# Kernel tuning notes

Measured on AMD Instinct MI355X. Metric: run time of the kernel, lower is better.

Reference implementation:

```python
import jax, jax.numpy as jnp
import numpy as np

N = 8192      # nodes
IN = 1433     # input_feat_dim
H1 = 256      # hidden_dim1
H2 = 128      # hidden_dim2
EPS = 1e-5    # BatchNorm1d eps
NEG = -9e15   # GAT mask value
SLOPE = 0.2   # leaky_relu negative slope (gamma)


def setup_inputs() -> dict:
    key = jax.random.key(0)
    ks = jax.random.split(key, 8)
    x = jax.random.normal(ks[0], (N, H2), dtype=jnp.float32)
    u = jax.random.uniform(ks[1], (N, N), dtype=jnp.float32)
    adj = jnp.where(u > 0.999, jnp.float32(0.01), jnp.float32(0.0))
    def w(k, shape):
        fan = shape[0]
        return jax.random.normal(k, shape, dtype=jnp.float32) / jnp.sqrt(jnp.float32(fan))
    return {
        "x": x,
        "adj": adj,
        "W_att": w(ks[2], (H2, H2)),
        "a_att": w(ks[3], (2 * H2, 1)),
        "W_fd1": w(ks[4], (H2, H1)),
        "bn1_g": jnp.ones((H1,), jnp.float32),
        "bn1_b": jnp.zeros((H1,), jnp.float32),
        "W_fd2": w(ks[5], (H1, IN)),
        "bn2_g": jnp.ones((IN,), jnp.float32),
        "bn2_b": jnp.zeros((IN,), jnp.float32),
        "W_sd1": w(ks[6], (H2, H1)),
        "bn3_g": jnp.ones((H1,), jnp.float32),
        "bn3_b": jnp.zeros((H1,), jnp.float32),
    }


def batchnorm(h, g, b):
    # BatchNorm1d training-mode forward: batch stats, biased variance
    m = h.mean(axis=0)
    v = ((h - m) ** 2).mean(axis=0)
    return (h - m) * jax.lax.rsqrt(v + EPS) * g + b


def reference(x, adj, W_att, a_att, W_fd1, bn1_g, bn1_b, W_fd2, bn2_g, bn2_b,
              W_sd1, bn3_g, bn3_b):
    # --- GraphAttentionLayer (concat=False, dropout=0) ---
    Wh = x @ W_att                       # [N, H2]
    f1 = Wh @ a_att[:H2]                 # [N, 1]
    f2 = Wh @ a_att[H2:]                 # [N, 1]
    e = jax.nn.leaky_relu(f1 + f2.T, SLOPE)          # [N, N]
    att = jnp.where(adj > 0, e, jnp.float32(NEG))
    att = jax.nn.softmax(att, axis=1)
    z = att @ Wh                         # condensed encoder output [N, H2]
    # --- feature decoder branch ---
    h1 = jax.nn.relu(adj @ (z @ W_fd1))  # GCN: adj @ (X W), relu
    h1 = batchnorm(h1, bn1_g, bn1_b)
    feat = jax.nn.relu(adj @ (h1 @ W_fd2))
    feat = batchnorm(feat, bn2_g, bn2_b)
    # --- structure decoder branch ---
    s1 = jax.nn.relu(adj @ (z @ W_sd1))
    s1 = batchnorm(s1, bn3_g, bn3_b)
    struct = s1 @ s1.T                   # inner-product decode, identity act [N, N]
    return feat, struct
```

## Files before the change

### kernel.cpp

```cpp
#include <hip/hip_runtime.h>
#include <hip/hip_bf16.h>
#include <stdint.h>

#define NN 8192
#define MAXNZ 64
#define BN_EPS 1e-5f
#define SLOPE 0.2f
#define IND 1433
#define NPAD 1536

typedef float f32x4v __attribute__((ext_vector_type(4)));
typedef short bf16x8v __attribute__((ext_vector_type(8)));

__device__ __forceinline__ float wave_sum(float v) {
#pragma unroll
  for (int off = 32; off > 0; off >>= 1) v += __shfl_xor(v, off);
  return v;
}
__device__ __forceinline__ float wave_max(float v) {
#pragma unroll
  for (int off = 32; off > 0; off >>= 1) v = fmaxf(v, __shfl_xor(v, off));
  return v;
}

#define GLOAD_LDS16(g, l)                                                      \
  __builtin_amdgcn_global_load_lds(                                            \
      (const __attribute__((address_space(1))) unsigned int*)(g),              \
      (__attribute__((address_space(3))) unsigned int*)(l), 16, 0, 0)

__global__ __launch_bounds__(256) void prep_gemm_k(
    const float* __restrict__ A, const float* __restrict__ B,
    const float* __restrict__ aatt, const float* __restrict__ W_fd2,
    const float* __restrict__ W_fd1, const float* __restrict__ W_sd1,
    __hip_bfloat16* __restrict__ Wt, __hip_bfloat16* __restrict__ Wcatb,
    float* __restrict__ C, float* __restrict__ cs, float* __restrict__ f1,
    float* __restrict__ f2) {
  __shared__ float As[64][68];
  __shared__ float Bs[64][68];
  __shared__ float csL[64];
  const int b = blockIdx.x;
  const int t = threadIdx.x;
  if (b < NPAD) {
    int o = b * 256 + t;
    int n = o >> 8, k = o & 255;
    Wt[o] = __float2bfloat16(n < IND ? W_fd2[(size_t)k * IND + n] : 0.f);
    if (b < 256) {
      int nn = o >> 7, kk = o & 127;
      float v = nn < 256 ? W_fd1[(size_t)kk * 256 + nn]
                         : W_sd1[(size_t)kk * 256 + (nn - 256)];
      Wcatb[o] = __float2bfloat16(v);
    }
    return;
  }
  const int bx = b - NPAD;
  const int m0 = (bx & 127) * 64, n0 = (bx >> 7) * 64;
  const int tx = t & 15, ty = t >> 4;
  if (t < 64) csL[t] = 0.f;
  float acc[4][4] = {};
  for (int kt = 0; kt < 128; kt += 64) {
    if (kt) __syncthreads();
#pragma unroll
    for (int i = 0; i < 4; ++i) {
      int fid = t + 256 * i;
      int r = fid >> 4, kq = (fid & 15) * 4;
      float4 v = *(const float4*)&A[(size_t)(m0 + r) * 128 + kt + kq];
      *(float4*)&As[r][kq] = v;
    }
#pragma unroll
    for (int i = 0; i < 4; ++i) {
      int fid = t + 256 * i;
      int r = fid >> 4, cq = (fid & 15) * 4;
      float4 v = *(const float4*)&B[(size_t)(kt + r) * 128 + n0 + cq];
      *(float4*)&Bs[r][cq] = v;
    }
    __syncthreads();
#pragma unroll 4
    for (int k0 = 0; k0 < 64; k0 += 4) {
      float4 a[4], bb[4];
#pragma unroll
      for (int i = 0; i < 4; ++i) a[i] = *(const float4*)&As[ty * 4 + i][k0];
#pragma unroll
      for (int j = 0; j < 4; ++j) bb[j] = *(const float4*)&Bs[k0 + j][tx * 4];
#pragma unroll
      for (int kk = 0; kk < 4; ++kk) {
#pragma unroll
        for (int i = 0; i < 4; ++i) {
          float av = ((const float*)&a[i])[kk];
#pragma unroll
          for (int j = 0; j < 4; ++j)
            acc[i][j] += av * ((const float*)&bb[kk])[j];
        }
      }
    }
  }
#pragma unroll
  for (int i = 0; i < 4; ++i) {
    float4 v = make_float4(acc[i][0], acc[i][1], acc[i][2], acc[i][3]);
    *(float4*)&C[(size_t)(m0 + ty * 4 + i) * 128 + n0 + tx * 4] = v;
  }
  float a1v[4], a2v[4];
#pragma unroll
  for (int j = 0; j < 4; ++j) {
    a1v[j] = aatt[n0 + tx * 4 + j];
    a2v[j] = aatt[128 + n0 + tx * 4 + j];
  }
#pragma unroll
  for (int i = 0; i < 4; ++i) {
    float p1 = acc[i][0] * a1v[0] + acc[i][1] * a1v[1] + acc[i][2] * a1v[2] +
               acc[i][3] * a1v[3];
    float p2 = acc[i][0] * a2v[0] + acc[i][1] * a2v[1] + acc[i][2] * a2v[2] +
               acc[i][3] * a2v[3];
#pragma unroll
    for (int off = 1; off < 16; off <<= 1) {
      p1 += __shfl_xor(p1, off);
      p2 += __shfl_xor(p2, off);
    }
    if ((t & 15) == 0) {
      atomicAdd(&f1[m0 + ty * 4 + i], p1);
      atomicAdd(&f2[m0 + ty * 4 + i], p2);
    }
  }
  float cp[4];
#pragma unroll
  for (int j = 0; j < 4; ++j) {
    cp[j] = acc[0][j] + acc[1][j] + acc[2][j] + acc[3][j];
    cp[j] += __shfl_xor(cp[j], 16);
    cp[j] += __shfl_xor(cp[j], 32);
  }
  if ((t & 63) < 16) {
#pragma unroll
    for (int j = 0; j < 4; ++j) atomicAdd(&csL[(t & 15) * 4 + j], cp[j]);
  }
  __syncthreads();
  if (t < 64) atomicAdd(&cs[n0 + t], csL[t]);
}

__global__ void extract_attn_k(const float* __restrict__ adj, const float* __restrict__ Wh,
                               const float* __restrict__ f1, const float* __restrict__ f2,
                               const float* __restrict__ cs, int* __restrict__ nnzA,
                               int* __restrict__ idxA, float* __restrict__ valA,
                               float* __restrict__ valsumA, float* __restrict__ z) {
  __shared__ int cntL[4];
  __shared__ int idxL[4][MAXNZ];
  __shared__ float valL[4][MAXNZ];
  int l = threadIdx.x & 63, w = threadIdx.x >> 6;
  int i = blockIdx.x * 4 + w;
  if (l == 0) cntL[w] = 0;
  const float* row = adj + (size_t)i * NN;
  for (int it = 0; it < NN / 512; ++it) {
    int c0 = it * 512 + l * 8;
    float4 va = *(const float4*)&row[c0];
    float4 vb = *(const float4*)&row[c0 + 4];
    float mx = fmaxf(fmaxf(fmaxf(va.x, va.y), fmaxf(va.z, va.w)),
                     fmaxf(fmaxf(vb.x, vb.y), fmaxf(vb.z, vb.w)));
    if (mx > 0.f) {
#pragma unroll
      for (int j = 0; j < 4; ++j) {
        float v = ((const float*)&va)[j];
        if (v > 0.f) {
          int s = atomicAdd(&cntL[w], 1);
          if (s < MAXNZ) { idxL[w][s] = c0 + j; valL[w][s] = v; }
        }
      }
#pragma unroll
      for (int j = 0; j < 4; ++j) {
        float v = ((const float*)&vb)[j];
        if (v > 0.f) {
          int s = atomicAdd(&cntL[w], 1);
          if (s < MAXNZ) { idxL[w][s] = c0 + 4 + j; valL[w][s] = v; }
        }
      }
    }
  }
  int nnz = cntL[w];
  nnz = nnz < MAXNZ ? nnz : MAXNZ;
  if (l == 0) nnzA[i] = nnz;

  int c = -1;
  float v = 0.f, att = 0.f;
  if (l < nnz) { c = idxL[w][l]; v = valL[w][l]; }
  idxA[(size_t)i * MAXNZ + l] = (l < nnz) ? c : 0;
  valA[(size_t)i * MAXNZ + l] = v;
  float vs = wave_sum(v);
  if (l == 0) valsumA[i] = vs;

  if (nnz == 0) {
    const float inv = 1.0f / 8192.0f;
    z[(size_t)i * 128 + l] = cs[l] * inv;
    z[(size_t)i * 128 + 64 + l] = cs[64 + l] * inv;
    return;
  }
  float e = -INFINITY;
  if (l < nnz) {
    float u = f1[i] + f2[c];
    e = u >= 0.f ? u : SLOPE * u;
  }
  float mx = wave_max(e);
  float p = (l < nnz) ? expf(e - mx) : 0.f;
  float s = wave_sum(p);
  att = p / s;
  float a0 = 0.f, a1 = 0.f;
  for (int j = 0; j < nnz; ++j) {
    float wt = __shfl(att, j);
    int r = __shfl(c, j);
    a0 += wt * Wh[(size_t)r * 128 + l];
    a1 += wt * Wh[(size_t)r * 128 + 64 + l];
  }
  z[(size_t)i * 128 + l] = a0;
  z[(size_t)i * 128 + 64 + l] = a1;
}

__global__ void gather_z_k(const float* __restrict__ X, const int* __restrict__ nnzA,
                           const int* __restrict__ idxA, const float* __restrict__ valA,
                           __hip_bfloat16* __restrict__ Y) {
  int l = threadIdx.x & 63, w = threadIdx.x >> 6;
  int i = blockIdx.x * 4 + w;
  int nnz = nnzA[i];
  int myi = idxA[(size_t)i * MAXNZ + l];
  float myv = valA[(size_t)i * MAXNZ + l];
  float a0 = 0.f, a1 = 0.f;
  for (int j = 0; j < nnz; ++j) {
    int r = __shfl(myi, j);
    float v = __shfl(myv, j);
    a0 += v * X[(size_t)r * 128 + l];
    a1 += v * X[(size_t)r * 128 + 64 + l];
  }
  Y[(size_t)i * 128 + l] = __float2bfloat16(a0);
  Y[(size_t)i * 128 + 64 + l] = __float2bfloat16(a1);
}

__global__ void s1_gather_k(const __hip_bfloat16* __restrict__ t, const int* __restrict__ nnzA,
                            const int* __restrict__ idxA, const float* __restrict__ valA,
                            const float* __restrict__ valsumA, const float* __restrict__ sums,
                            const float* __restrict__ sumsq, const float* __restrict__ g1,
                            const float* __restrict__ b1, const float* __restrict__ g3,
                            const float* __restrict__ b3, __hip_bfloat16* __restrict__ s1b,
                            __hip_bfloat16* __restrict__ ghb) {
  __shared__ int idxL[MAXNZ];
  __shared__ float valL[MAXNZ];
  int i = blockIdx.x, tt = threadIdx.x;
  int nnz = nnzA[i];
  if (tt < MAXNZ) {
    idxL[tt] = idxA[(size_t)i * MAXNZ + tt];
    valL[tt] = valA[(size_t)i * MAXNZ + tt];
  }
  __syncthreads();
  {
    float m = sums[256 + tt] * (1.f / 8192.f);
    float va = fmaxf(sumsq[256 + tt] * (1.f / 8192.f) - m * m, 0.f);
    float sc = g3[tt] * rsqrtf(va + BN_EPS);
    float sh = b3[tt] - m * sc;
    float v = __bfloat162float(t[(size_t)i * 512 + 256 + tt]) * sc + sh;
    s1b[(size_t)i * 256 + tt] = __float2bfloat16(v);
  }
  float acc = 0.f;
  for (int j = 0; j < nnz; ++j)
    acc += valL[j] * __bfloat162float(t[(size_t)idxL[j] * 512 + tt]);
  float m = sums[tt] * (1.f / 8192.f);
  float va = fmaxf(sumsq[tt] * (1.f / 8192.f) - m * m, 0.f);
  float sc = g1[tt] * rsqrtf(va + BN_EPS);
  float sh = b1[tt] - m * sc;
  ghb[(size_t)i * 256 + tt] = __float2bfloat16(acc * sc + sh * valsumA[i]);
}

__global__ void feat_apply_k(const __hip_bfloat16* __restrict__ fp, const float* __restrict__ sums,
                             const float* __restrict__ sumsq, const float* __restrict__ g,
                             const float* __restrict__ b, float* __restrict__ out) {
  int i = blockIdx.x;
  for (int c = threadIdx.x; c < IND; c += 256) {
    float m = sums[c] * (1.f / 8192.f);
    float va = fmaxf(sumsq[c] * (1.f / 8192.f) - m * m, 0.f);
    float sc = g[c] * rsqrtf(va + BN_EPS);
    float sh = b[c] - m * sc;
    out[(size_t)i * IND + c] = __bfloat162float(fp[(size_t)i * NPAD + c]) * sc + sh;
  }
}

template <int KT>
__global__ __launch_bounds__(256) void mfma_bt_k(const short* __restrict__ A,
                                                 const short* __restrict__ Bt,
                                                 __hip_bfloat16* __restrict__ C, int ldc,
                                                 int gridN, float* __restrict__ sums,
                                                 float* __restrict__ sumsq) {
  __shared__ short lds[2][16384];
  const int nwg = gridDim.x;
  const int cpx = nwg >> 3;
  const int bid = blockIdx.x;
  const int wg = (bid & 7) * cpx + (bid >> 3);
  const int m0 = (wg / gridN) * 128, n0 = (wg % gridN) * 128;
  const int t = threadIdx.x;
  const int l = t & 63, w = t >> 6;
  const int wm = w >> 1, wn = w & 1;
  const int KW = KT * 128;
  f32x4v acc[4][4];
#pragma unroll
  for (int i = 0; i < 4; ++i)
#pragma unroll
    for (int j = 0; j < 4; ++j)
#pragma unroll
      for (int q = 0; q < 4; ++q) acc[i][j][q] = 0.f;

  for (int kt = 0; kt < KT; ++kt) {
    if (kt) __syncthreads();
#pragma unroll
    for (int i = 0; i < 8; ++i) {
      int region = w * 8 + i;
      int lr = region * 4 + (l >> 4);
      int ch = (l & 15) ^ (lr & 7);
      const short* gA = A + ((size_t)(m0 + lr) * KW + kt * 128 + ch * 8);
      GLOAD_LDS16(gA, &lds[0][region * 512]);
      const short* gB = Bt + ((size_t)(n0 + lr) * KW + kt * 128 + ch * 8);
      GLOAD_LDS16(gB, &lds[1][region * 512]);
    }
    __syncthreads();
#pragma unroll
    for (int ks = 0; ks < 4; ++ks) {
      bf16x8v af[4], bf[4];
#pragma unroll
      for (int mi = 0; mi < 4; ++mi) {
        int lr = wm * 64 + mi * 16 + (l & 15);
        int ch = (ks * 4 + (l >> 4)) ^ (lr & 7);
        af[mi] = *(const bf16x8v*)&lds[0][lr * 128 + ch * 8];
      }
#pragma unroll
      for (int nj = 0; nj < 4; ++nj) {
        int lr = wn * 64 + nj * 16 + (l & 15);
        int ch = (ks * 4 + (l >> 4)) ^ (lr & 7);
        bf[nj] = *(const bf16x8v*)&lds[1][lr * 128 + ch * 8];
      }
#pragma unroll
      for (int mi = 0; mi < 4; ++mi)
#pragma unroll
        for (int nj = 0; nj < 4; ++nj)
          acc[mi][nj] = __builtin_amdgcn_mfma_f32_16x16x32_bf16(
              af[mi], bf[nj], acc[mi][nj], 0, 0, 0);
    }
  }
#pragma unroll
  for (int nj = 0; nj < 4; ++nj) {
    int col = n0 + wn * 64 + nj * 16 + (l & 15);
    float s = 0.f, ss = 0.f;
#pragma unroll
    for (int mi = 0; mi < 4; ++mi) {
#pragma unroll
      for (int q = 0; q < 4; ++q) {
        int row = m0 + wm * 64 + mi * 16 + (l >> 4) * 4 + q;
        float v = fmaxf(acc[mi][nj][q], 0.f);
        C[(size_t)row * ldc + col] = __float2bfloat16(v);
        s += v;
        ss += v * v;
      }
    }
    s += __shfl_xor(s, 16);
    s += __shfl_xor(s, 32);
    ss += __shfl_xor(ss, 16);
    ss += __shfl_xor(ss, 32);
    if ((l >> 4) == 0) {
      atomicAdd(&sums[col], s);
      atomicAdd(&sumsq[col], ss);
    }
  }
}

__global__ __launch_bounds__(256) void tail_k(const short* __restrict__ Agh,
                                              const short* __restrict__ Wt,
                                              __hip_bfloat16* __restrict__ featb,
                                              float* __restrict__ sums,
                                              float* __restrict__ sumsq,
                                              const short* __restrict__ S,
                                              float* __restrict__ C) {
  __shared__ short lds[2][16384];
  const int bid = blockIdx.x;
  const int fA = bid * 24 / 89;
  const int fB = (bid + 1) * 24 / 89;
  const bool isFeat = fB > fA;
  const int t = threadIdx.x;
  const int l = t & 63, w = t >> 6;
  const int wm = w >> 1, wn = w & 1;
  f32x4v acc[4][4];
#pragma unroll
  for (int i = 0; i < 4; ++i)
#pragma unroll
    for (int j = 0; j < 4; ++j)
#pragma unroll
      for (int q = 0; q < 4; ++q) acc[i][j][q] = 0.f;

  if (isFeat) {
    const int fb = fA;
    const int wg = (fb & 7) * 96 + (fb >> 3);
    const int m0 = (wg / 12) * 128, n0 = (wg % 12) * 128;
    for (int kt = 0; kt < 2; ++kt) {
      if (kt) __syncthreads();
#pragma unroll
      for (int i = 0; i < 8; ++i) {
        int region = w * 8 + i;
        int lr = region * 4 + (l >> 4);
        int ch = (l & 15) ^ (lr & 7);
        const short* gA = Agh + ((size_t)(m0 + lr) * 256 + kt * 128 + ch * 8);
        GLOAD_LDS16(gA, &lds[0][region * 512]);
        const short* gB = Wt + ((size_t)(n0 + lr) * 256 + kt * 128 + ch * 8);
        GLOAD_LDS16(gB, &lds[1][region * 512]);
      }
      __syncthreads();
#pragma unroll
      for (int ks = 0; ks < 4; ++ks) {
        bf16x8v af[4], bf[4];
#pragma unroll
        for (int mi = 0; mi < 4; ++mi) {
          int lr = wm * 64 + mi * 16 + (l & 15);
          int ch = (ks * 4 + (l >> 4)) ^ (lr & 7);
          af[mi] = *(const bf16x8v*)&lds[0][lr * 128 + ch * 8];
        }
#pragma unroll
        for (int nj = 0; nj < 4; ++nj) {
          int lr = wn * 64 + nj * 16 + (l & 15);
          int ch = (ks * 4 + (l >> 4)) ^ (lr & 7);
          bf[nj] = *(const bf16x8v*)&lds[1][lr * 128 + ch * 8];
        }
#pragma unroll
        for (int mi = 0; mi < 4; ++mi)
#pragma unroll
          for (int nj = 0; nj < 4; ++nj)
            acc[mi][nj] = __builtin_amdgcn_mfma_f32_16x16x32_bf16(
                af[mi], bf[nj], acc[mi][nj], 0, 0, 0);
      }
    }
#pragma unroll
    for (int nj = 0; nj < 4; ++nj) {
      int col = n0 + wn * 64 + nj * 16 + (l & 15);
      float s = 0.f, ss = 0.f;
#pragma unroll
      for (int mi = 0; mi < 4; ++mi) {
#pragma unroll
        for (int q = 0; q < 4; ++q) {
          int row = m0 + wm * 64 + mi * 16 + (l >> 4) * 4 + q;
          float v = fmaxf(acc[mi][nj][q], 0.f);
          featb[(size_t)row * NPAD + col] = __float2bfloat16(v);
          s += v;
          ss += v * v;
        }
      }
      s += __shfl_xor(s, 16);
      s += __shfl_xor(s, 32);
      ss += __shfl_xor(ss, 16);
      ss += __shfl_xor(ss, 32);
      if ((l >> 4) == 0) {
        atomicAdd(&sums[col], s);
        atomicAdd(&sumsq[col], ss);
      }
    }
  } else {
    const int sb = bid - fA;
    const int wg = (sb & 7) * 260 + (sb >> 3);
    int bi = (int)((129.0f - sqrtf(16641.0f - 8.0f * (float)wg)) * 0.5f);
    while ((bi + 1) * 64 - ((bi + 1) * bi) / 2 <= wg) ++bi;
    while (bi * 64 - (bi * (bi - 1)) / 2 > wg) --bi;
    const int bj = bi + (wg - (bi * 64 - (bi * (bi - 1)) / 2));
    const int m0 = bi * 128, n0 = bj * 128;
    for (int kt = 0; kt < 2; ++kt) {
      if (kt) __syncthreads();
#pragma unroll
      for (int i = 0; i < 8; ++i) {
        int region = w * 8 + i;
        int lr = region * 4 + (l >> 4);
        int ch = (l & 15) ^ (lr & 7);
        const short* gA = S + ((size_t)(m0 + lr) * 256 + kt * 128 + ch * 8);
        GLOAD_LDS16(gA, &lds[0][region * 512]);
        const short* gB = S + ((size_t)(n0 + lr) * 256 + kt * 128 + ch * 8);
        GLOAD_LDS16(gB, &lds[1][region * 512]);
      }
      __syncthreads();
#pragma unroll
      for (int ks = 0; ks < 4; ++ks) {
        bf16x8v af[4], bf[4];
#pragma unroll
        for (int mi = 0; mi < 4; ++mi) {
          int lr = wm * 64 + mi * 16 + (l & 15);
          int ch = (ks * 4 + (l >> 4)) ^ (lr & 7);
          af[mi] = *(const bf16x8v*)&lds[0][lr * 128 + ch * 8];
        }
#pragma unroll
        for (int nj = 0; nj < 4; ++nj) {
          int lr = wn * 64 + nj * 16 + (l & 15);
          int ch = (ks * 4 + (l >> 4)) ^ (lr & 7);
          bf[nj] = *(const bf16x8v*)&lds[1][lr * 128 + ch * 8];
        }
#pragma unroll
        for (int mi = 0; mi < 4; ++mi)
#pragma unroll
          for (int nj = 0; nj < 4; ++nj)
            acc[mi][nj] = __builtin_amdgcn_mfma_f32_16x16x32_bf16(
                af[mi], bf[nj], acc[mi][nj], 0, 0, 0);
      }
    }
#pragma unroll
    for (int mi = 0; mi < 4; ++mi) {
#pragma unroll
      for (int nj = 0; nj < 4; ++nj) {
        int col = n0 + wn * 64 + nj * 16 + (l & 15);
#pragma unroll
        for (int q = 0; q < 4; ++q) {
          int row = m0 + wm * 64 + mi * 16 + (l >> 4) * 4 + q;
          C[(size_t)row * NN + col] = acc[mi][nj][q];
        }
      }
    }
    if (bi != bj) {
#pragma unroll
      for (int nj = 0; nj < 4; ++nj) {
        int col = n0 + wn * 64 + nj * 16 + (l & 15);
#pragma unroll
        for (int mi = 0; mi < 4; ++mi) {
          int row0 = m0 + wm * 64 + mi * 16 + (l >> 4) * 4;
          float4 v = make_float4(acc[mi][nj][0], acc[mi][nj][1], acc[mi][nj][2],
                                 acc[mi][nj][3]);
          *(float4*)&C[(size_t)col * NN + row0] = v;
        }
      }
    }
  }
}

extern "C" void kernel_launch(void* const* d_in, const int* in_sizes, int n_in,
                              void* d_out, int out_size, void* d_ws, size_t ws_size,
                              hipStream_t stream) {
  const float* x = (const float*)d_in[0];
  const float* adj = (const float*)d_in[1];
  const float* W_att = (const float*)d_in[2];
  const float* a_att = (const float*)d_in[3];
  const float* W_fd1 = (const float*)d_in[4];
  const float* bn1g = (const float*)d_in[5];
  const float* bn1b = (const float*)d_in[6];
  const float* W_fd2 = (const float*)d_in[7];
  const float* bn2g = (const float*)d_in[8];
  const float* bn2b = (const float*)d_in[9];
  const float* W_sd1 = (const float*)d_in[10];
  const float* bn3g = (const float*)d_in[11];
  const float* bn3b = (const float*)d_in[12];

  float* out = (float*)d_out;
  float* feat_out = out;
  float* struct_out = out + (size_t)NN * IND;

  float* ws = (float*)d_ws;
  size_t off = 0;
  auto alloc = [&](size_t nfloats) {
    float* p = ws + off;
    off += (nfloats + 255) & ~(size_t)255;
    return p;
  };
  float* Wh = alloc((size_t)NN * 128);
  float* z = alloc((size_t)NN * 128);
  float* valsum = alloc(NN);
  const size_t ZTOT = 256 + 8192 + 8192 + 512 + 512 + 1536 + 1536;
  float* zbase = alloc(ZTOT);
  float* cs = zbase;
  float* f1 = zbase + 256;
  float* f2 = zbase + 256 + 8192;
  float* sumsA = zbase + 256 + 16384;
  float* sumsqA = sumsA + 512;
  float* sumsB = sumsqA + 512;
  float* sumsqB = sumsB + 1536;
  float* valA = alloc((size_t)NN * MAXNZ);
  int* idxA = (int*)alloc((size_t)NN * MAXNZ);
  int* nnzA = (int*)alloc(NN);
  __hip_bfloat16* tbuf = (__hip_bfloat16*)alloc((size_t)NN * 256);
  __hip_bfloat16* gb = (__hip_bfloat16*)alloc((size_t)NN * 64);
  __hip_bfloat16* s1b = (__hip_bfloat16*)alloc((size_t)NN * 128);
  __hip_bfloat16* ghb = (__hip_bfloat16*)alloc((size_t)NN * 128);
  __hip_bfloat16* Wt = (__hip_bfloat16*)alloc((size_t)NPAD * 128);
  __hip_bfloat16* Wcatb = (__hip_bfloat16*)alloc(512 * 64);
  __hip_bfloat16* featb = (__hip_bfloat16*)alloc((size_t)NN * NPAD / 2);

  hipMemsetAsync(zbase, 0, ZTOT * sizeof(float), stream);

  prep_gemm_k<<<NPAD + 256, 256, 0, stream>>>(x, W_att, a_att, W_fd2, W_fd1, W_sd1,
                                              Wt, Wcatb, Wh, cs, f1, f2);

  extract_attn_k<<<NN / 4, 256, 0, stream>>>(adj, Wh, f1, f2, cs, nnzA, idxA, valA,
                                             valsum, z);
  gather_z_k<<<NN / 4, 256, 0, stream>>>(z, nnzA, idxA, valA, gb);

  mfma_bt_k<1><<<64 * 4, 256, 0, stream>>>((const short*)gb, (const short*)Wcatb,
                                           tbuf, 512, 4, sumsA, sumsqA);
  s1_gather_k<<<NN, 256, 0, stream>>>(tbuf, nnzA, idxA, valA, valsum, sumsA, sumsqA,
                                      bn1g, bn1b, bn3g, bn3b, s1b, ghb);

  tail_k<<<2848, 256, 0, stream>>>((const short*)ghb, (const short*)Wt, featb,
                                   sumsB, sumsqB, (const short*)s1b, struct_out);
  feat_apply_k<<<NN, 256, 0, stream>>>(featb, sumsB, sumsqB, bn2g, bn2b, feat_out);
}
```

Measured before the change: 249.7 us.

## Fuse all stages into one persistent kernel with software grid barriers

Replaces the seven separate kernel launches with a single persistent kernel of 512 blocks. Each block loops over the work items of every former stage, and atomic-counter grid barriers separate the stages. The aim is to remove launch gaps and tail idle time between the small stages. In exchange, correctness depends on all 512 blocks being co-resident, barrier spinning adds cost, and the fixed grid size may leave the large GEMM and adjacency-scan phases less parallel.

```diff
diff --git a/kernel.cpp b/kernel.cpp
--- a/kernel.cpp
+++ b/kernel.cpp
@@ -8,6 +8,7 @@
 #define SLOPE 0.2f
 #define IND 1433
 #define NPAD 1536
+#define NBLK 512
 
 typedef float f32x4v __attribute__((ext_vector_type(4)));
 typedef short bf16x8v __attribute__((ext_vector_type(8)));
@@ -28,289 +29,273 @@
       (const __attribute__((address_space(1))) unsigned int*)(g),              \
       (__attribute__((address_space(3))) unsigned int*)(l), 16, 0, 0)
 
-__global__ __launch_bounds__(256) void prep_gemm_k(
-    const float* __restrict__ A, const float* __restrict__ B,
-    const float* __restrict__ aatt, const float* __restrict__ W_fd2,
-    const float* __restrict__ W_fd1, const float* __restrict__ W_sd1,
+__device__ __forceinline__ void grid_bar(int* bar, int target) {
+  __syncthreads();
+  if (threadIdx.x == 0) {
+    __threadfence();
+    __hip_atomic_fetch_add(bar, 1, __ATOMIC_ACQ_REL, __HIP_MEMORY_SCOPE_AGENT);
+    while (__hip_atomic_load(bar, __ATOMIC_ACQUIRE, __HIP_MEMORY_SCOPE_AGENT) <
+           target)
+      __builtin_amdgcn_s_sleep(2);
+    __threadfence();
+  }
+  __syncthreads();
+}
+
+__global__ __launch_bounds__(256, 2) void mega_k(
+    const float* __restrict__ x, const float* __restrict__ adj,
+    const float* __restrict__ W_att, const float* __restrict__ a_att,
+    const float* __restrict__ W_fd1, const float* __restrict__ bn1g,
+    const float* __restrict__ bn1b, const float* __restrict__ W_fd2,
+    const float* __restrict__ bn2g, const float* __restrict__ bn2b,
+    const float* __restrict__ W_sd1, const float* __restrict__ bn3g,
+    const float* __restrict__ bn3b, float* __restrict__ feat_out,
+    float* __restrict__ struct_out, float* __restrict__ Wh,
+    float* __restrict__ z, float* __restrict__ valsum, int* __restrict__ bar,
+    float* __restrict__ cs, float* __restrict__ f1, float* __restrict__ f2,
+    float* __restrict__ sumsA, float* __restrict__ sumsqA,
+    float* __restrict__ sumsB, float* __restrict__ sumsqB,
+    float* __restrict__ valA, int* __restrict__ idxA, int* __restrict__ nnzA,
+    __hip_bfloat16* __restrict__ tbuf, __hip_bfloat16* __restrict__ gb,
+    __hip_bfloat16* __restrict__ s1b, __hip_bfloat16* __restrict__ ghb,
     __hip_bfloat16* __restrict__ Wt, __hip_bfloat16* __restrict__ Wcatb,
-    float* __restrict__ C, float* __restrict__ cs, float* __restrict__ f1,
-    float* __restrict__ f2) {
-  __shared__ float As[64][68];
-  __shared__ float Bs[64][68];
-  __shared__ float csL[64];
-  const int b = blockIdx.x;
-  const int t = threadIdx.x;
-  if (b < NPAD) {
-    int o = b * 256 + t;
-    int n = o >> 8, k = o & 255;
-    Wt[o] = __float2bfloat16(n < IND ? W_fd2[(size_t)k * IND + n] : 0.f);
-    if (b < 256) {
-      int nn = o >> 7, kk = o & 127;
-      float v = nn < 256 ? W_fd1[(size_t)kk * 256 + nn]
-                         : W_sd1[(size_t)kk * 256 + (nn - 256)];
-      Wcatb[o] = __float2bfloat16(v);
-    }
-    return;
-  }
-  const int bx = b - NPAD;
-  const int m0 = (bx & 127) * 64, n0 = (bx >> 7) * 64;
-  const int tx = t & 15, ty = t >> 4;
-  if (t < 64) csL[t] = 0.f;
-  float acc[4][4] = {};
-  for (int kt = 0; kt < 128; kt += 64) {
-    if (kt) __syncthreads();
-#pragma unroll
-    for (int i = 0; i < 4; ++i) {
-      int fid = t + 256 * i;
-      int r = fid >> 4, kq = (fid & 15) * 4;
-      float4 v = *(const float4*)&A[(size_t)(m0 + r) * 128 + kt + kq];
-      *(float4*)&As[r][kq] = v;
-    }
-#pragma unroll
-    for (int i = 0; i < 4; ++i) {
-      int fid = t + 256 * i;
-      int r = fid >> 4, cq = (fid & 15) * 4;
-      float4 v = *(const float4*)&B[(size_t)(kt + r) * 128 + n0 + cq];
-      *(float4*)&Bs[r][cq] = v;
-    }
-    __syncthreads();
-#pragma unroll 4
-    for (int k0 = 0; k0 < 64; k0 += 4) {
-      float4 a[4], bb[4];
-#pragma unroll
-      for (int i = 0; i < 4; ++i) a[i] = *(const float4*)&As[ty * 4 + i][k0];
-#pragma unroll
-      for (int j = 0; j < 4; ++j) bb[j] = *(const float4*)&Bs[k0 + j][tx * 4];
-#pragma unroll
-      for (int kk = 0; kk < 4; ++kk) {
-#pragma unroll
-        for (int i = 0; i < 4; ++i) {
-          float av = ((const float*)&a[i])[kk];
-#pragma unroll
-          for (int j = 0; j < 4; ++j)
-            acc[i][j] += av * ((const float*)&bb[kk])[j];
-        }
-      }
-    }
-  }
-#pragma unroll
-  for (int i = 0; i < 4; ++i) {
-    float4 v = make_float4(acc[i][0], acc[i][1], acc[i][2], acc[i][3]);
-    *(float4*)&C[(size_t)(m0 + ty * 4 + i) * 128 + n0 + tx * 4] = v;
-  }
-  float a1v[4], a2v[4];
-#pragma unroll
-  for (int j = 0; j < 4; ++j) {
-    a1v[j] = aatt[n0 + tx * 4 + j];
-    a2v[j] = aatt[128 + n0 + tx * 4 + j];
-  }
-#pragma unroll
-  for (int i = 0; i < 4; ++i) {
-    float p1 = acc[i][0] * a1v[0] + acc[i][1] * a1v[1] + acc[i][2] * a1v[2] +
-               acc[i][3] * a1v[3];
-    float p2 = acc[i][0] * a2v[0] + acc[i][1] * a2v[1] + acc[i][2] * a2v[2] +
-               acc[i][3] * a2v[3];
-#pragma unroll
-    for (int off = 1; off < 16; off <<= 1) {
-      p1 += __shfl_xor(p1, off);
-      p2 += __shfl_xor(p2, off);
-    }
-    if ((t & 15) == 0) {
-      atomicAdd(&f1[m0 + ty * 4 + i], p1);
-      atomicAdd(&f2[m0 + ty * 4 + i], p2);
-    }
-  }
-  float cp[4];
-#pragma unroll
-  for (int j = 0; j < 4; ++j) {
-    cp[j] = acc[0][j] + acc[1][j] + acc[2][j] + acc[3][j];
-    cp[j] += __shfl_xor(cp[j], 16);
-    cp[j] += __shfl_xor(cp[j], 32);
-  }
-  if ((t & 63) < 16) {
-#pragma unroll
-    for (int j = 0; j < 4; ++j) atomicAdd(&csL[(t & 15) * 4 + j], cp[j]);
-  }
-  __syncthreads();
-  if (t < 64) atomicAdd(&cs[n0 + t], csL[t]);
-}
-
-__global__ void extract_attn_k(const float* __restrict__ adj, const float* __restrict__ Wh,
-                               const float* __restrict__ f1, const float* __restrict__ f2,
-                               const float* __restrict__ cs, int* __restrict__ nnzA,
-                               int* __restrict__ idxA, float* __restrict__ valA,
-                               float* __restrict__ valsumA, float* __restrict__ z) {
-  __shared__ int cntL[4];
-  __shared__ int idxL[4][MAXNZ];
-  __shared__ float valL[4][MAXNZ];
-  int l = threadIdx.x & 63, w = threadIdx.x >> 6;
-  int i = blockIdx.x * 4 + w;
-  if (l == 0) cntL[w] = 0;
-  const float* row = adj + (size_t)i * NN;
-  for (int it = 0; it < NN / 512; ++it) {
-    int c0 = it * 512 + l * 8;
-    float4 va = *(const float4*)&row[c0];
-    float4 vb = *(const float4*)&row[c0 + 4];
-    float mx = fmaxf(fmaxf(fmaxf(va.x, va.y), fmaxf(va.z, va.w)),
-                     fmaxf(fmaxf(vb.x, vb.y), fmaxf(vb.z, vb.w)));
-    if (mx > 0.f) {
-#pragma unroll
-      for (int j = 0; j < 4; ++j) {
-        float v = ((const float*)&va)[j];
-        if (v > 0.f) {
-          int s = atomicAdd(&cntL[w], 1);
-          if (s < MAXNZ) { idxL[w][s] = c0 + j; valL[w][s] = v; }
-        }
-      }
-#pragma unroll
-      for (int j = 0; j < 4; ++j) {
-        float v = ((const float*)&vb)[j];
-        if (v > 0.f) {
-          int s = atomicAdd(&cntL[w], 1);
-          if (s < MAXNZ) { idxL[w][s] = c0 + 4 + j; valL[w][s] = v; }
-        }
-      }
-    }
-  }
-  int nnz = cntL[w];
-  nnz = nnz < MAXNZ ? nnz : MAXNZ;
-  if (l == 0) nnzA[i] = nnz;
-
-  int c = -1;
-  float v = 0.f, att = 0.f;
-  if (l < nnz) { c = idxL[w][l]; v = valL[w][l]; }
-  idxA[(size_t)i * MAXNZ + l] = (l < nnz) ? c : 0;
-  valA[(size_t)i * MAXNZ + l] = v;
-  float vs = wave_sum(v);
-  if (l == 0) valsumA[i] = vs;
-
-  if (nnz == 0) {
-    const float inv = 1.0f / 8192.0f;
-    z[(size_t)i * 128 + l] = cs[l] * inv;
-    z[(size_t)i * 128 + 64 + l] = cs[64 + l] * inv;
-    return;
-  }
-  float e = -INFINITY;
-  if (l < nnz) {
-    float u = f1[i] + f2[c];
-    e = u >= 0.f ? u : SLOPE * u;
-  }
-  float mx = wave_max(e);
-  float p = (l < nnz) ? expf(e - mx) : 0.f;
-  float s = wave_sum(p);
-  att = p / s;
-  float a0 = 0.f, a1 = 0.f;
-  for (int j = 0; j < nnz; ++j) {
-    float wt = __shfl(att, j);
-    int r = __shfl(c, j);
-    a0 += wt * Wh[(size_t)r * 128 + l];
-    a1 += wt * Wh[(size_t)r * 128 + 64 + l];
-  }
-  z[(size_t)i * 128 + l] = a0;
-  z[(size_t)i * 128 + 64 + l] = a1;
-}
-
-__global__ void gather_z_k(const float* __restrict__ X, const int* __restrict__ nnzA,
-                           const int* __restrict__ idxA, const float* __restrict__ valA,
-                           __hip_bfloat16* __restrict__ Y) {
-  int l = threadIdx.x & 63, w = threadIdx.x >> 6;
-  int i = blockIdx.x * 4 + w;
-  int nnz = nnzA[i];
-  int myi = idxA[(size_t)i * MAXNZ + l];
-  float myv = valA[(size_t)i * MAXNZ + l];
-  float a0 = 0.f, a1 = 0.f;
-  for (int j = 0; j < nnz; ++j) {
-    int r = __shfl(myi, j);
-    float v = __shfl(myv, j);
-    a0 += v * X[(size_t)r * 128 + l];
-    a1 += v * X[(size_t)r * 128 + 64 + l];
-  }
-  Y[(size_t)i * 128 + l] = __float2bfloat16(a0);
-  Y[(size_t)i * 128 + 64 + l] = __float2bfloat16(a1);
-}
-
-__global__ void s1_gather_k(const __hip_bfloat16* __restrict__ t, const int* __restrict__ nnzA,
-                            const int* __restrict__ idxA, const float* __restrict__ valA,
-                            const float* __restrict__ valsumA, const float* __restrict__ sums,
-                            const float* __restrict__ sumsq, const float* __restrict__ g1,
-                            const float* __restrict__ b1, const float* __restrict__ g3,
-                            const float* __restrict__ b3, __hip_bfloat16* __restrict__ s1b,
-                            __hip_bfloat16* __restrict__ ghb) {
-  __shared__ int idxL[MAXNZ];
-  __shared__ float valL[MAXNZ];
-  int i = blockIdx.x, tt = threadIdx.x;
-  int nnz = nnzA[i];
-  if (tt < MAXNZ) {
-    idxL[tt] = idxA[(size_t)i * MAXNZ + tt];
-    valL[tt] = valA[(size_t)i * MAXNZ + tt];
-  }
-  __syncthreads();
-  {
-    float m = sums[256 + tt] * (1.f / 8192.f);
-    float va = fmaxf(sumsq[256 + tt] * (1.f / 8192.f) - m * m, 0.f);
-    float sc = g3[tt] * rsqrtf(va + BN_EPS);
-    float sh = b3[tt] - m * sc;
-    float v = __bfloat162float(t[(size_t)i * 512 + 256 + tt]) * sc + sh;
-    s1b[(size_t)i * 256 + tt] = __float2bfloat16(v);
-  }
-  float acc = 0.f;
-  for (int j = 0; j < nnz; ++j)
-    acc += valL[j] * __bfloat162float(t[(size_t)idxL[j] * 512 + tt]);
-  float m = sums[tt] * (1.f / 8192.f);
-  float va = fmaxf(sumsq[tt] * (1.f / 8192.f) - m * m, 0.f);
-  float sc = g1[tt] * rsqrtf(va + BN_EPS);
-  float sh = b1[tt] - m * sc;
-  ghb[(size_t)i * 256 + tt] = __float2bfloat16(acc * sc + sh * valsumA[i]);
-}
-
-__global__ void feat_apply_k(const __hip_bfloat16* __restrict__ fp, const float* __restrict__ sums,
-                             const float* __restrict__ sumsq, const float* __restrict__ g,
-                             const float* __restrict__ b, float* __restrict__ out) {
-  int i = blockIdx.x;
-  for (int c = threadIdx.x; c < IND; c += 256) {
-    float m = sums[c] * (1.f / 8192.f);
-    float va = fmaxf(sumsq[c] * (1.f / 8192.f) - m * m, 0.f);
-    float sc = g[c] * rsqrtf(va + BN_EPS);
-    float sh = b[c] - m * sc;
-    out[(size_t)i * IND + c] = __bfloat162float(fp[(size_t)i * NPAD + c]) * sc + sh;
-  }
-}
-
-template <int KT>
-__global__ __launch_bounds__(256) void mfma_bt_k(const short* __restrict__ A,
-                                                 const short* __restrict__ Bt,
-                                                 __hip_bfloat16* __restrict__ C, int ldc,
-                                                 int gridN, float* __restrict__ sums,
-                                                 float* __restrict__ sumsq) {
-  __shared__ short lds[2][16384];
-  const int nwg = gridDim.x;
-  const int cpx = nwg >> 3;
-  const int bid = blockIdx.x;
-  const int wg = (bid & 7) * cpx + (bid >> 3);
-  const int m0 = (wg / gridN) * 128, n0 = (wg % gridN) * 128;
+    __hip_bfloat16* __restrict__ featb) {
+  __shared__ union ShMem {
+    short stag[2][16384];
+    struct {
+      float As[64][68];
+      float Bs[64][68];
+      float csL[64];
+    } g0;
+    struct {
+      int cnt[4];
+      int idx[4][MAXNZ];
+      float val[4][MAXNZ];
+    } ex;
+    struct {
+      int idx[MAXNZ];
+      float val[MAXNZ];
+    } sg;
+  } sh;
+
   const int t = threadIdx.x;
   const int l = t & 63, w = t >> 6;
-  const int wm = w >> 1, wn = w & 1;
-  const int KW = KT * 128;
-  f32x4v acc[4][4];
-#pragma unroll
-  for (int i = 0; i < 4; ++i)
-#pragma unroll
-    for (int j = 0; j < 4; ++j)
-#pragma unroll
-      for (int q = 0; q < 4; ++q) acc[i][j][q] = 0.f;
-
-  for (int kt = 0; kt < KT; ++kt) {
-    if (kt) __syncthreads();
+
+  for (int job = blockIdx.x; job < NPAD + 256; job += NBLK) {
+    if (job < NPAD) {
+      int o = job * 256 + t;
+      int n = o >> 8, k = o & 255;
+      Wt[o] = __float2bfloat16(n < IND ? W_fd2[(size_t)k * IND + n] : 0.f);
+      if (job < 256) {
+        int nn = o >> 7, kk = o & 127;
+        float v = nn < 256 ? W_fd1[(size_t)kk * 256 + nn]
+                           : W_sd1[(size_t)kk * 256 + (nn - 256)];
+        Wcatb[o] = __float2bfloat16(v);
+      }
+    } else {
+      const int bx = job - NPAD;
+      const int m0 = (bx & 127) * 64, n0 = (bx >> 7) * 64;
+      const int tx = t & 15, ty = t >> 4;
+      __syncthreads();
+      if (t < 64) sh.g0.csL[t] = 0.f;
+      float acc[4][4] = {};
+      for (int kt = 0; kt < 128; kt += 64) {
+        if (kt) __syncthreads();
+#pragma unroll
+        for (int i = 0; i < 4; ++i) {
+          int fid = t + 256 * i;
+          int r = fid >> 4, kq = (fid & 15) * 4;
+          float4 v = *(const float4*)&x[(size_t)(m0 + r) * 128 + kt + kq];
+          *(float4*)&sh.g0.As[r][kq] = v;
+        }
+#pragma unroll
+        for (int i = 0; i < 4; ++i) {
+          int fid = t + 256 * i;
+          int r = fid >> 4, cq = (fid & 15) * 4;
+          float4 v = *(const float4*)&W_att[(size_t)(kt + r) * 128 + n0 + cq];
+          *(float4*)&sh.g0.Bs[r][cq] = v;
+        }
+        __syncthreads();
+#pragma unroll 4
+        for (int k0 = 0; k0 < 64; k0 += 4) {
+          float4 a[4], bb[4];
+#pragma unroll
+          for (int i = 0; i < 4; ++i)
+            a[i] = *(const float4*)&sh.g0.As[ty * 4 + i][k0];
+#pragma unroll
+          for (int j = 0; j < 4; ++j)
+            bb[j] = *(const float4*)&sh.g0.Bs[k0 + j][tx * 4];
+#pragma unroll
+          for (int kk = 0; kk < 4; ++kk) {
+#pragma unroll
+            for (int i = 0; i < 4; ++i) {
+              float av = ((const float*)&a[i])[kk];
+#pragma unroll
+              for (int j = 0; j < 4; ++j)
+                acc[i][j] += av * ((const float*)&bb[kk])[j];
+            }
+          }
+        }
+      }
+#pragma unroll
+      for (int i = 0; i < 4; ++i) {
+        float4 v = make_float4(acc[i][0], acc[i][1], acc[i][2], acc[i][3]);
+        *(float4*)&Wh[(size_t)(m0 + ty * 4 + i) * 128 + n0 + tx * 4] = v;
+      }
+      float a1v[4], a2v[4];
+#pragma unroll
+      for (int j = 0; j < 4; ++j) {
+        a1v[j] = a_att[n0 + tx * 4 + j];
+        a2v[j] = a_att[128 + n0 + tx * 4 + j];
+      }
+#pragma unroll
+      for (int i = 0; i < 4; ++i) {
+        float p1 = acc[i][0] * a1v[0] + acc[i][1] * a1v[1] +
+                   acc[i][2] * a1v[2] + acc[i][3] * a1v[3];
+        float p2 = acc[i][0] * a2v[0] + acc[i][1] * a2v[1] +
+                   acc[i][2] * a2v[2] + acc[i][3] * a2v[3];
+#pragma unroll
+        for (int off = 1; off < 16; off <<= 1) {
+          p1 += __shfl_xor(p1, off);
+          p2 += __shfl_xor(p2, off);
+        }
+        if ((t & 15) == 0) {
+          atomicAdd(&f1[m0 + ty * 4 + i], p1);
+          atomicAdd(&f2[m0 + ty * 4 + i], p2);
+        }
+      }
+      float cp[4];
+#pragma unroll
+      for (int j = 0; j < 4; ++j) {
+        cp[j] = acc[0][j] + acc[1][j] + acc[2][j] + acc[3][j];
+        cp[j] += __shfl_xor(cp[j], 16);
+        cp[j] += __shfl_xor(cp[j], 32);
+      }
+      if ((t & 63) < 16) {
+#pragma unroll
+        for (int j = 0; j < 4; ++j)
+          atomicAdd(&sh.g0.csL[(t & 15) * 4 + j], cp[j]);
+      }
+      __syncthreads();
+      if (t < 64) atomicAdd(&cs[n0 + t], sh.g0.csL[t]);
+      __syncthreads();
+    }
+  }
+  grid_bar(bar, NBLK);
+
+  {
+    auto push4 = [&](const float4& vv, int base) {
+#pragma unroll
+      for (int j = 0; j < 4; ++j) {
+        float pv = ((const float*)&vv)[j];
+        if (pv > 0.f) {
+          int s = atomicAdd(&sh.ex.cnt[w], 1);
+          if (s < MAXNZ) {
+            sh.ex.idx[w][s] = base + j;
+            sh.ex.val[w][s] = pv;
+          }
+        }
+      }
+    };
+    for (int rj = 0; rj < 4; ++rj) {
+      const int i = blockIdx.x * 4 + w + rj * 2048;
+      if (l == 0) sh.ex.cnt[w] = 0;
+      const float* row = adj + (size_t)i * NN;
+      for (int it = 0; it < 8; ++it) {
+        int c0 = it * 1024 + l * 16;
+        float4 v0 = *(const float4*)&row[c0];
+        float4 v1 = *(const float4*)&row[c0 + 4];
+        float4 v2 = *(const float4*)&row[c0 + 8];
+        float4 v3 = *(const float4*)&row[c0 + 12];
+        float m01 = fmaxf(fmaxf(fmaxf(v0.x, v0.y), fmaxf(v0.z, v0.w)),
+                          fmaxf(fmaxf(v1.x, v1.y), fmaxf(v1.z, v1.w)));
+        float m23 = fmaxf(fmaxf(fmaxf(v2.x, v2.y), fmaxf(v2.z, v2.w)),
+                          fmaxf(fmaxf(v3.x, v3.y), fmaxf(v3.z, v3.w)));
+        if (fmaxf(m01, m23) > 0.f) {
+          push4(v0, c0);
+          push4(v1, c0 + 4);
+          push4(v2, c0 + 8);
+          push4(v3, c0 + 12);
+        }
+      }
+      int nnz = sh.ex.cnt[w];
+      nnz = nnz < MAXNZ ? nnz : MAXNZ;
+      if (l == 0) nnzA[i] = nnz;
+      int c = -1;
+      float v = 0.f;
+      if (l < nnz) {
+        c = sh.ex.idx[w][l];
+        v = sh.ex.val[w][l];
+      }
+      idxA[(size_t)i * MAXNZ + l] = (l < nnz) ? c : 0;
+      valA[(size_t)i * MAXNZ + l] = v;
+      float vs = wave_sum(v);
+      if (l == 0) valsum[i] = vs;
+      if (nnz == 0) {
+        const float inv = 1.0f / 8192.0f;
+        z[(size_t)i * 128 + l] = cs[l] * inv;
+        z[(size_t)i * 128 + 64 + l] = cs[64 + l] * inv;
+        continue;
+      }
+      float e = -INFINITY;
+      if (l < nnz) {
+        float u = f1[i] + f2[c];
+        e = u >= 0.f ? u : SLOPE * u;
+      }
+      float mx = wave_max(e);
+      float p = (l < nnz) ? expf(e - mx) : 0.f;
+      float s = wave_sum(p);
+      float att = p / s;
+      float a0 = 0.f, a1 = 0.f;
+      for (int j = 0; j < nnz; ++j) {
+        float wt = __shfl(att, j);
+        int r = __shfl(c, j);
+        a0 += wt * Wh[(size_t)r * 128 + l];
+        a1 += wt * Wh[(size_t)r * 128 + 64 + l];
+      }
+      z[(size_t)i * 128 + l] = a0;
+      z[(size_t)i * 128 + 64 + l] = a1;
+    }
+  }
+  grid_bar(bar, 2 * NBLK);
+
+  for (int rj = 0; rj < 4; ++rj) {
+    const int i = blockIdx.x * 4 + w + rj * 2048;
+    int nnz = nnzA[i];
+    int myi = idxA[(size_t)i * MAXNZ + l];
+    float myv = valA[(size_t)i * MAXNZ + l];
+    float a0 = 0.f, a1 = 0.f;
+    for (int j = 0; j < nnz; ++j) {
+      int r = __shfl(myi, j);
+      float v = __shfl(myv, j);
+      a0 += v * z[(size_t)r * 128 + l];
+      a1 += v * z[(size_t)r * 128 + 64 + l];
+    }
+    gb[(size_t)i * 128 + l] = __float2bfloat16(a0);
+    gb[(size_t)i * 128 + 64 + l] = __float2bfloat16(a1);
+  }
+  grid_bar(bar, 3 * NBLK);
+
+  if (blockIdx.x < 256) {
+    const int wg = blockIdx.x;
+    const int m0 = (wg >> 2) * 128, n0 = (wg & 3) * 128;
+    const int wm = w >> 1, wn = w & 1;
+    f32x4v acc[4][4];
+#pragma unroll
+    for (int i = 0; i < 4; ++i)
+#pragma unroll
+      for (int j = 0; j < 4; ++j)
+#pragma unroll
+        for (int q = 0; q < 4; ++q) acc[i][j][q] = 0.f;
 #pragma unroll
     for (int i = 0; i < 8; ++i) {
       int region = w * 8 + i;
       int lr = region * 4 + (l >> 4);
       int ch = (l & 15) ^ (lr & 7);
-      const short* gA = A + ((size_t)(m0 + lr) * KW + kt * 128 + ch * 8);
-      GLOAD_LDS16(gA, &lds[0][region * 512]);
-      const short* gB = Bt + ((size_t)(n0 + lr) * KW + kt * 128 + ch * 8);
-      GLOAD_LDS16(gB, &lds[1][region * 512]);
+      const short* gA = (const short*)gb + ((size_t)(m0 + lr) * 128 + ch * 8);
+      GLOAD_LDS16(gA, &sh.stag[0][region * 512]);
+      const short* gB = (const short*)Wcatb + ((size_t)(n0 + lr) * 128 + ch * 8);
+      GLOAD_LDS16(gB, &sh.stag[1][region * 512]);
     }
     __syncthreads();
 #pragma unroll
@@ -320,13 +305,13 @@
       for (int mi = 0; mi < 4; ++mi) {
         int lr = wm * 64 + mi * 16 + (l & 15);
         int ch = (ks * 4 + (l >> 4)) ^ (lr & 7);
-        af[mi] = *(const bf16x8v*)&lds[0][lr * 128 + ch * 8];
+        af[mi] = *(const bf16x8v*)&sh.stag[0][lr * 128 + ch * 8];
       }
 #pragma unroll
       for (int nj = 0; nj < 4; ++nj) {
         int lr = wn * 64 + nj * 16 + (l & 15);
         int ch = (ks * 4 + (l >> 4)) ^ (lr & 7);
-        bf[nj] = *(const bf16x8v*)&lds[1][lr * 128 + ch * 8];
+        bf[nj] = *(const bf16x8v*)&sh.stag[1][lr * 128 + ch * 8];
       }
 #pragma unroll
       for (int mi = 0; mi < 4; ++mi)
@@ -335,96 +320,6 @@
           acc[mi][nj] = __builtin_amdgcn_mfma_f32_16x16x32_bf16(
               af[mi], bf[nj], acc[mi][nj], 0, 0, 0);
     }
-  }
-#pragma unroll
-  for (int nj = 0; nj < 4; ++nj) {
-    int col = n0 + wn * 64 + nj * 16 + (l & 15);
-    float s = 0.f, ss = 0.f;
-#pragma unroll
-    for (int mi = 0; mi < 4; ++mi) {
-#pragma unroll
-      for (int q = 0; q < 4; ++q) {
-        int row = m0 + wm * 64 + mi * 16 + (l >> 4) * 4 + q;
-        float v = fmaxf(acc[mi][nj][q], 0.f);
-        C[(size_t)row * ldc + col] = __float2bfloat16(v);
-        s += v;
-        ss += v * v;
-      }
-    }
-    s += __shfl_xor(s, 16);
-    s += __shfl_xor(s, 32);
-    ss += __shfl_xor(ss, 16);
-    ss += __shfl_xor(ss, 32);
-    if ((l >> 4) == 0) {
-      atomicAdd(&sums[col], s);
-      atomicAdd(&sumsq[col], ss);
-    }
-  }
-}
-
-__global__ __launch_bounds__(256) void tail_k(const short* __restrict__ Agh,
-                                              const short* __restrict__ Wt,
-                                              __hip_bfloat16* __restrict__ featb,
-                                              float* __restrict__ sums,
-                                              float* __restrict__ sumsq,
-                                              const short* __restrict__ S,
-                                              float* __restrict__ C) {
-  __shared__ short lds[2][16384];
-  const int bid = blockIdx.x;
-  const int fA = bid * 24 / 89;
-  const int fB = (bid + 1) * 24 / 89;
-  const bool isFeat = fB > fA;
-  const int t = threadIdx.x;
-  const int l = t & 63, w = t >> 6;
-  const int wm = w >> 1, wn = w & 1;
-  f32x4v acc[4][4];
-#pragma unroll
-  for (int i = 0; i < 4; ++i)
-#pragma unroll
-    for (int j = 0; j < 4; ++j)
-#pragma unroll
-      for (int q = 0; q < 4; ++q) acc[i][j][q] = 0.f;
-
-  if (isFeat) {
-    const int fb = fA;
-    const int wg = (fb & 7) * 96 + (fb >> 3);
-    const int m0 = (wg / 12) * 128, n0 = (wg % 12) * 128;
-    for (int kt = 0; kt < 2; ++kt) {
-      if (kt) __syncthreads();
-#pragma unroll
-      for (int i = 0; i < 8; ++i) {
-        int region = w * 8 + i;
-        int lr = region * 4 + (l >> 4);
-        int ch = (l & 15) ^ (lr & 7);
-        const short* gA = Agh + ((size_t)(m0 + lr) * 256 + kt * 128 + ch * 8);
-        GLOAD_LDS16(gA, &lds[0][region * 512]);
-        const short* gB = Wt + ((size_t)(n0 + lr) * 256 + kt * 128 + ch * 8);
-        GLOAD_LDS16(gB, &lds[1][region * 512]);
-      }
-      __syncthreads();
-#pragma unroll
-      for (int ks = 0; ks < 4; ++ks) {
-        bf16x8v af[4], bf[4];
-#pragma unroll
-        for (int mi = 0; mi < 4; ++mi) {
-          int lr = wm * 64 + mi * 16 + (l & 15);
-          int ch = (ks * 4 + (l >> 4)) ^ (lr & 7);
-          af[mi] = *(const bf16x8v*)&lds[0][lr * 128 + ch * 8];
-        }
-#pragma unroll
-        for (int nj = 0; nj < 4; ++nj) {
-          int lr = wn * 64 + nj * 16 + (l & 15);
-          int ch = (ks * 4 + (l >> 4)) ^ (lr & 7);
-          bf[nj] = *(const bf16x8v*)&lds[1][lr * 128 + ch * 8];
-        }
-#pragma unroll
-        for (int mi = 0; mi < 4; ++mi)
-#pragma unroll
-          for (int nj = 0; nj < 4; ++nj)
-            acc[mi][nj] = __builtin_amdgcn_mfma_f32_16x16x32_bf16(
-                af[mi], bf[nj], acc[mi][nj], 0, 0, 0);
-      }
-    }
 #pragma unroll
     for (int nj = 0; nj < 4; ++nj) {
       int col = n0 + wn * 64 + nj * 16 + (l & 15);
@@ -435,7 +330,7 @@
         for (int q = 0; q < 4; ++q) {
           int row = m0 + wm * 64 + mi * 16 + (l >> 4) * 4 + q;
           float v = fmaxf(acc[mi][nj][q], 0.f);
-          featb[(size_t)row * NPAD + col] = __float2bfloat16(v);
+          tbuf[(size_t)row * 512 + col] = __float2bfloat16(v);
           s += v;
           ss += v * v;
         }
@@ -445,77 +340,215 @@
       ss += __shfl_xor(ss, 16);
       ss += __shfl_xor(ss, 32);
       if ((l >> 4) == 0) {
-        atomicAdd(&sums[col], s);
-        atomicAdd(&sumsq[col], ss);
-      }
-    }
-  } else {
-    const int sb = bid - fA;
-    const int wg = (sb & 7) * 260 + (sb >> 3);
-    int bi = (int)((129.0f - sqrtf(16641.0f - 8.0f * (float)wg)) * 0.5f);
-    while ((bi + 1) * 64 - ((bi + 1) * bi) / 2 <= wg) ++bi;
-    while (bi * 64 - (bi * (bi - 1)) / 2 > wg) --bi;
-    const int bj = bi + (wg - (bi * 64 - (bi * (bi - 1)) / 2));
-    const int m0 = bi * 128, n0 = bj * 128;
-    for (int kt = 0; kt < 2; ++kt) {
-      if (kt) __syncthreads();
-#pragma unroll
-      for (int i = 0; i < 8; ++i) {
-        int region = w * 8 + i;
-        int lr = region * 4 + (l >> 4);
-        int ch = (l & 15) ^ (lr & 7);
-        const short* gA = S + ((size_t)(m0 + lr) * 256 + kt * 128 + ch * 8);
-        GLOAD_LDS16(gA, &lds[0][region * 512]);
-        const short* gB = S + ((size_t)(n0 + lr) * 256 + kt * 128 + ch * 8);
-        GLOAD_LDS16(gB, &lds[1][region * 512]);
-      }
+        atomicAdd(&sumsA[col], s);
+        atomicAdd(&sumsqA[col], ss);
+      }
+    }
+  }
+  grid_bar(bar, 4 * NBLK);
+
+  {
+    float m1 = sumsA[t] * (1.f / 8192.f);
+    float va1 = fmaxf(sumsqA[t] * (1.f / 8192.f) - m1 * m1, 0.f);
+    float sc1 = bn1g[t] * rsqrtf(va1 + BN_EPS);
+    float sh1 = bn1b[t] - m1 * sc1;
+    float m3 = sumsA[256 + t] * (1.f / 8192.f);
+    float va3 = fmaxf(sumsqA[256 + t] * (1.f / 8192.f) - m3 * m3, 0.f);
+    float sc3 = bn3g[t] * rsqrtf(va3 + BN_EPS);
+    float sh3 = bn3b[t] - m3 * sc3;
+    for (int rj = 0; rj < 16; ++rj) {
+      const int i = blockIdx.x + rj * NBLK;
+      int nnz = nnzA[i];
       __syncthreads();
-#pragma unroll
-      for (int ks = 0; ks < 4; ++ks) {
-        bf16x8v af[4], bf[4];
-#pragma unroll
-        for (int mi = 0; mi < 4; ++mi) {
-          int lr = wm * 64 + mi * 16 + (l & 15);
-          int ch = (ks * 4 + (l >> 4)) ^ (lr & 7);
-          af[mi] = *(const bf16x8v*)&lds[0][lr * 128 + ch * 8];
-        }
-#pragma unroll
-        for (int nj = 0; nj < 4; ++nj) {
-          int lr = wn * 64 + nj * 16 + (l & 15);
-          int ch = (ks * 4 + (l >> 4)) ^ (lr & 7);
-          bf[nj] = *(const bf16x8v*)&lds[1][lr * 128 + ch * 8];
-        }
-#pragma unroll
-        for (int mi = 0; mi < 4; ++mi)
-#pragma unroll
-          for (int nj = 0; nj < 4; ++nj)
-            acc[mi][nj] = __builtin_amdgcn_mfma_f32_16x16x32_bf16(
-                af[mi], bf[nj], acc[mi][nj], 0, 0, 0);
-      }
-    }
-#pragma unroll
-    for (int mi = 0; mi < 4; ++mi) {
+      if (t < MAXNZ) {
+        sh.sg.idx[t] = idxA[(size_t)i * MAXNZ + t];
+        sh.sg.val[t] = valA[(size_t)i * MAXNZ + t];
+      }
+      __syncthreads();
+      float v3 = __bfloat162float(tbuf[(size_t)i * 512 + 256 + t]) * sc3 + sh3;
+      s1b[(size_t)i * 256 + t] = __float2bfloat16(v3);
+      float acc = 0.f;
+      for (int j = 0; j < nnz; ++j)
+        acc += sh.sg.val[j] * __bfloat162float(tbuf[(size_t)sh.sg.idx[j] * 512 + t]);
+      ghb[(size_t)i * 256 + t] = __float2bfloat16(acc * sc1 + sh1 * valsum[i]);
+    }
+  }
+  grid_bar(bar, 5 * NBLK);
+
+  for (int job = blockIdx.x; job < 2848; job += NBLK) {
+    __syncthreads();
+    const int fA = job * 24 / 89;
+    const bool isFeat = ((job + 1) * 24 / 89) > fA;
+    const int wm = w >> 1, wn = w & 1;
+    f32x4v acc[4][4];
+#pragma unroll
+    for (int i = 0; i < 4; ++i)
+#pragma unroll
+      for (int j = 0; j < 4; ++j)
+#pragma unroll
+        for (int q = 0; q < 4; ++q) acc[i][j][q] = 0.f;
+
+    if (isFeat) {
+      const int fb = fA;
+      const int wg = (fb & 7) * 96 + (fb >> 3);
+      const int m0 = (wg / 12) * 128, n0 = (wg % 12) * 128;
+      for (int kt = 0; kt < 2; ++kt) {
+        if (kt) __syncthreads();
+#pragma unroll
+        for (int i = 0; i < 8; ++i) {
+          int region = w * 8 + i;
+          int lr = region * 4 + (l >> 4);
+          int ch = (l & 15) ^ (lr & 7);
+          const short* gA =
+              (const short*)ghb + ((size_t)(m0 + lr) * 256 + kt * 128 + ch * 8);
+          GLOAD_LDS16(gA, &sh.stag[0][region * 512]);
+          const short* gB =
+              (const short*)Wt + ((size_t)(n0 + lr) * 256 + kt * 128 + ch * 8);
+          GLOAD_LDS16(gB, &sh.stag[1][region * 512]);
+        }
+        __syncthreads();
+#pragma unroll
+        for (int ks = 0; ks < 4; ++ks) {
+          bf16x8v af[4], bf[4];
+#pragma unroll
+          for (int mi = 0; mi < 4; ++mi) {
+            int lr = wm * 64 + mi * 16 + (l & 15);
+            int ch = (ks * 4 + (l >> 4)) ^ (lr & 7);
+            af[mi] = *(const bf16x8v*)&sh.stag[0][lr * 128 + ch * 8];
+          }
+#pragma unroll
+          for (int nj = 0; nj < 4; ++nj) {
+            int lr = wn * 64 + nj * 16 + (l & 15);
+            int ch = (ks * 4 + (l >> 4)) ^ (lr & 7);
+            bf[nj] = *(const bf16x8v*)&sh.stag[1][lr * 128 + ch * 8];
+          }
+#pragma unroll
+          for (int mi = 0; mi < 4; ++mi)
+#pragma unroll
+            for (int nj = 0; nj < 4; ++nj)
+              acc[mi][nj] = __builtin_amdgcn_mfma_f32_16x16x32_bf16(
+                  af[mi], bf[nj], acc[mi][nj], 0, 0, 0);
+        }
+      }
 #pragma unroll
       for (int nj = 0; nj < 4; ++nj) {
         int col = n0 + wn * 64 + nj * 16 + (l & 15);
-#pragma unroll
-        for (int q = 0; q < 4; ++q) {
-          int row = m0 + wm * 64 + mi * 16 + (l >> 4) * 4 + q;
-          C[(size_t)row * NN + col] = acc[mi][nj][q];
-        }
-      }
-    }
-    if (bi != bj) {
-#pragma unroll
-      for (int nj = 0; nj < 4; ++nj) {
-        int col = n0 + wn * 64 + nj * 16 + (l & 15);
+        float s = 0.f, ss = 0.f;
 #pragma unroll
         for (int mi = 0; mi < 4; ++mi) {
-          int row0 = m0 + wm * 64 + mi * 16 + (l >> 4) * 4;
-          float4 v = make_float4(acc[mi][nj][0], acc[mi][nj][1], acc[mi][nj][2],
-                                 acc[mi][nj][3]);
-          *(float4*)&C[(size_t)col * NN + row0] = v;
-        }
+#pragma unroll
+          for (int q = 0; q < 4; ++q) {
+            int row = m0 + wm * 64 + mi * 16 + (l >> 4) * 4 + q;
+            float v = fmaxf(acc[mi][nj][q], 0.f);
+            featb[(size_t)row * NPAD + col] = __float2bfloat16(v);
+            s += v;
+            ss += v * v;
+          }
+        }
+        s += __shfl_xor(s, 16);
+        s += __shfl_xor(s, 32);
+        ss += __shfl_xor(ss, 16);
+        ss += __shfl_xor(ss, 32);
+        if ((l >> 4) == 0) {
+          atomicAdd(&sumsB[col], s);
+          atomicAdd(&sumsqB[col], ss);
+        }
+      }
+    } else {
+      const int sb = job - fA;
+      const int wg = (sb & 7) * 260 + (sb >> 3);
+      int bi = (int)((129.0f - sqrtf(16641.0f - 8.0f * (float)wg)) * 0.5f);
+      while ((bi + 1) * 64 - ((bi + 1) * bi) / 2 <= wg) ++bi;
+      while (bi * 64 - (bi * (bi - 1)) / 2 > wg) --bi;
+      const int bj = bi + (wg - (bi * 64 - (bi * (bi - 1)) / 2));
+      const int m0 = bi * 128, n0 = bj * 128;
+      for (int kt = 0; kt < 2; ++kt) {
+        if (kt) __syncthreads();
+#pragma unroll
+        for (int i = 0; i < 8; ++i) {
+          int region = w * 8 + i;
+          int lr = region * 4 + (l >> 4);
+          int ch = (l & 15) ^ (lr & 7);
+          const short* gA =
+              (const short*)s1b + ((size_t)(m0 + lr) * 256 + kt * 128 + ch * 8);
+          GLOAD_LDS16(gA, &sh.stag[0][region * 512]);
+          const short* gB =
+              (const short*)s1b + ((size_t)(n0 + lr) * 256 + kt * 128 + ch * 8);
+          GLOAD_LDS16(gB, &sh.stag[1][region * 512]);
+        }
+        __syncthreads();
+#pragma unroll
+        for (int ks = 0; ks < 4; ++ks) {
+          bf16x8v af[4], bf[4];
+#pragma unroll
+          for (int mi = 0; mi < 4; ++mi) {
+            int lr = wm * 64 + mi * 16 + (l & 15);
+            int ch = (ks * 4 + (l >> 4)) ^ (lr & 7);
+            af[mi] = *(const bf16x8v*)&sh.stag[0][lr * 128 + ch * 8];
+          }
+#pragma unroll
+          for (int nj = 0; nj < 4; ++nj) {
+            int lr = wn * 64 + nj * 16 + (l & 15);
+            int ch = (ks * 4 + (l >> 4)) ^ (lr & 7);
+            bf[nj] = *(const bf16x8v*)&sh.stag[1][lr * 128 + ch * 8];
+          }
+#pragma unroll
+          for (int mi = 0; mi < 4; ++mi)
+#pragma unroll
+            for (int nj = 0; nj < 4; ++nj)
+              acc[mi][nj] = __builtin_amdgcn_mfma_f32_16x16x32_bf16(
+                  af[mi], bf[nj], acc[mi][nj], 0, 0, 0);
+        }
+      }
+#pragma unroll
+      for (int mi = 0; mi < 4; ++mi) {
+#pragma unroll
+        for (int nj = 0; nj < 4; ++nj) {
+          int col = n0 + wn * 64 + nj * 16 + (l & 15);
+#pragma unroll
+          for (int q = 0; q < 4; ++q) {
+            int row = m0 + wm * 64 + mi * 16 + (l >> 4) * 4 + q;
+            struct_out[(size_t)row * NN + col] = acc[mi][nj][q];
+          }
+        }
+      }
+      if (bi != bj) {
+#pragma unroll
+        for (int nj = 0; nj < 4; ++nj) {
+          int col = n0 + wn * 64 + nj * 16 + (l & 15);
+#pragma unroll
+          for (int mi = 0; mi < 4; ++mi) {
+            int row0 = m0 + wm * 64 + mi * 16 + (l >> 4) * 4;
+            float4 v = make_float4(acc[mi][nj][0], acc[mi][nj][1],
+                                   acc[mi][nj][2], acc[mi][nj][3]);
+            *(float4*)&struct_out[(size_t)col * NN + row0] = v;
+          }
+        }
+      }
+    }
+  }
+  grid_bar(bar, 6 * NBLK);
+
+  {
+    float sc[6], shf[6];
+#pragma unroll
+    for (int q = 0; q < 6; ++q) {
+      int c = t + q * 256;
+      if (c < IND) {
+        float m = sumsB[c] * (1.f / 8192.f);
+        float va = fmaxf(sumsqB[c] * (1.f / 8192.f) - m * m, 0.f);
+        sc[q] = bn2g[c] * rsqrtf(va + BN_EPS);
+        shf[q] = bn2b[c] - m * sc[q];
+      }
+    }
+    for (int rj = 0; rj < 16; ++rj) {
+      const int i = blockIdx.x + rj * NBLK;
+#pragma unroll
+      for (int q = 0; q < 6; ++q) {
+        int c = t + q * 256;
+        if (c < IND)
+          feat_out[(size_t)i * IND + c] =
+              __bfloat162float(featb[(size_t)i * NPAD + c]) * sc[q] + shf[q];
       }
     }
   }
@@ -552,12 +585,13 @@
   float* Wh = alloc((size_t)NN * 128);
   float* z = alloc((size_t)NN * 128);
   float* valsum = alloc(NN);
-  const size_t ZTOT = 256 + 8192 + 8192 + 512 + 512 + 1536 + 1536;
+  const size_t ZTOT = 256 + 256 + 8192 + 8192 + 512 + 512 + 1536 + 1536;
   float* zbase = alloc(ZTOT);
-  float* cs = zbase;
-  float* f1 = zbase + 256;
-  float* f2 = zbase + 256 + 8192;
-  float* sumsA = zbase + 256 + 16384;
+  int* bar = (int*)zbase;
+  float* cs = zbase + 256;
+  float* f1 = zbase + 512;
+  float* f2 = f1 + 8192;
+  float* sumsA = f2 + 8192;
   float* sumsqA = sumsA + 512;
   float* sumsB = sumsqA + 512;
   float* sumsqB = sumsB + 1536;
@@ -574,19 +608,9 @@
 
   hipMemsetAsync(zbase, 0, ZTOT * sizeof(float), stream);
 
-  prep_gemm_k<<<NPAD + 256, 256, 0, stream>>>(x, W_att, a_att, W_fd2, W_fd1, W_sd1,
-                                              Wt, Wcatb, Wh, cs, f1, f2);
-
-  extract_attn_k<<<NN / 4, 256, 0, stream>>>(adj, Wh, f1, f2, cs, nnzA, idxA, valA,
-                                             valsum, z);
-  gather_z_k<<<NN / 4, 256, 0, stream>>>(z, nnzA, idxA, valA, gb);
-
-  mfma_bt_k<1><<<64 * 4, 256, 0, stream>>>((const short*)gb, (const short*)Wcatb,
-                                           tbuf, 512, 4, sumsA, sumsqA);
-  s1_gather_k<<<NN, 256, 0, stream>>>(tbuf, nnzA, idxA, valA, valsum, sumsA, sumsqA,
-                                      bn1g, bn1b, bn3g, bn3b, s1b, ghb);
-
-  tail_k<<<2848, 256, 0, stream>>>((const short*)ghb, (const short*)Wt, featb,
-                                   sumsB, sumsqB, (const short*)s1b, struct_out);
-  feat_apply_k<<<NN, 256, 0, stream>>>(featb, sumsB, sumsqB, bn2g, bn2b, feat_out);
+  mega_k<<<NBLK, 256, 0, stream>>>(
+      x, adj, W_att, a_att, W_fd1, bn1g, bn1b, W_fd2, bn2g, bn2b, W_sd1, bn3g,
+      bn3b, feat_out, struct_out, Wh, z, valsum, bar, cs, f1, f2, sumsA,
+      sumsqA, sumsB, sumsqB, valA, idxA, nnzA, tbuf, gb, s1b, ghb, Wt, Wcatb,
+      featb);
 }
```

Result: slower. 897.9 us (+259.5%).
